# Kernel optimization log

Measured on AMD Instinct MI355X. Metric: run time of the kernel, lower is better.

Reference implementation:

```python
import jax, jax.numpy as jnp
import numpy as np

B, S, D_MODEL, D_K, D_V, H = 4, 2048, 1024, 1024, 1024, 16


def setup_inputs() -> dict:
    key = jax.random.key(0)
    ks = jax.random.split(key, 8)
    std_qk = np.sqrt(2.0 / (D_MODEL + D_K)).astype(np.float32)
    std_v = np.sqrt(2.0 / (D_MODEL + D_V)).astype(np.float32)
    std_o = np.sqrt(2.0 / (D_V + D_MODEL)).astype(np.float32)  # xavier normal
    return {
        "Q": jax.random.normal(ks[0], (B, S, D_MODEL), jnp.float32),
        "K": jax.random.normal(ks[1], (B, S, D_MODEL), jnp.float32),
        "V": jax.random.normal(ks[2], (B, S, D_MODEL), jnp.float32),
        "Wq": jax.random.normal(ks[3], (D_MODEL, D_K), jnp.float32) * std_qk,
        "bq": jnp.zeros((D_K,), jnp.float32),
        "Wk": jax.random.normal(ks[4], (D_MODEL, D_K), jnp.float32) * std_qk,
        "bk": jnp.zeros((D_K,), jnp.float32),
        "Wv": jax.random.normal(ks[5], (D_MODEL, D_V), jnp.float32) * std_v,
        "bv": jnp.zeros((D_V,), jnp.float32),
        "Wo": jax.random.normal(ks[6], (D_V, D_MODEL), jnp.float32) * std_o,
        "bo": jnp.zeros((D_MODEL,), jnp.float32),
    }


def reference(Q, K, V, Wq, bq, Wk, bk, Wv, bv, Wo, bo):
    b, s, _ = Q.shape
    hd = D_K // H  # per-head dim
    # separate QKV projections
    q = (Q @ Wq + bq).reshape(b, s, H, hd)
    k = (K @ Wk + bk).reshape(b, s, H, hd)
    v = (V @ Wv + bv).reshape(b, s, H, D_V // H)
    # scaled dot-product attention per head
    scale = 1.0 / jnp.sqrt(jnp.asarray(hd, Q.dtype))
    scores = jnp.einsum("bqhd,bkhd->bhqk", q, k) * scale
    attn = jax.nn.softmax(scores, axis=-1)
    o = jnp.einsum("bhqk,bkhd->bqhd", attn, v).reshape(b, s, D_V)
    # output projection
    return o @ Wo + bo
```

## Files before the change

kernel.cpp:

```cpp
#include <hip/hip_runtime.h>
#include <hip/hip_bf16.h>
#include <stdint.h>


#define B_  4
#define S_  2048
#define DM  1024
#define H_  16
#define HD  64
#define BH  (B_ * H_)

typedef __attribute__((ext_vector_type(8))) short short8;
typedef __attribute__((ext_vector_type(4))) float f32x4;

union U8 { short8 v; ushort u[8]; };

__device__ __forceinline__ ushort f2bf(float f) {
  union { float f; uint32_t i; } x; x.f = f;
  uint32_t r = (x.i + 0x7FFFu + ((x.i >> 16) & 1u)) >> 16;
  return (ushort)r;
}

__device__ __forceinline__ uint32_t cvt_pk_bf16(float a, float b) {
  uint32_t r;
  asm("v_cvt_pk_bf16_f32 %0, %1, %2" : "=v"(r) : "v"(a), "v"(b));
  return r;
}

__device__ __forceinline__ float exp2f_fast(float x) {
  float r;
  asm("v_exp_f32 %0, %1" : "=v"(r) : "v"(x));
  return r;
}

__device__ __forceinline__ void glds16(const ushort* g, ushort* l) {
  __builtin_amdgcn_global_load_lds(
      (const __attribute__((address_space(1))) void*)g,
      (__attribute__((address_space(3))) void*)l, 16, 0, 0);
}

#define MAX3(a, b, c) fmaxf(fmaxf((a), (b)), (c))

__global__ __launch_bounds__(256) void transposeW4(
    const float* __restrict__ s0, const float* __restrict__ s1,
    const float* __restrict__ s2, const float* __restrict__ s3,
    ushort* __restrict__ dbase) {
  __shared__ __align__(16) ushort tile[64][72];
  const int t = threadIdx.x;
  const int bx = blockIdx.x & 15;
  const int by = blockIdx.x >> 4;
  const int wsel = blockIdx.y;
  const float* src = wsel == 0 ? s0 : (wsel == 1 ? s1 : (wsel == 2 ? s2 : s3));
  ushort* dst = dbase + (size_t)wsel * 1024 * 1024;
#pragma unroll
  for (int i = 0; i < 2; i++) {
    int e = (i * 256 + t) * 8;
    int r = e >> 6, c = e & 63;
    const float* sp = src + (size_t)(by * 64 + r) * 1024 + bx * 64 + c;
    float4 a = ((const float4*)sp)[0];
    float4 b = ((const float4*)sp)[1];
    tile[r][c + 0] = f2bf(a.x); tile[r][c + 1] = f2bf(a.y);
    tile[r][c + 2] = f2bf(a.z); tile[r][c + 3] = f2bf(a.w);
    tile[r][c + 4] = f2bf(b.x); tile[r][c + 5] = f2bf(b.y);
    tile[r][c + 6] = f2bf(b.z); tile[r][c + 7] = f2bf(b.w);
  }
  __syncthreads();
#pragma unroll
  for (int i = 0; i < 2; i++) {
    int e = (i * 256 + t) * 8;
    int r = e >> 6, c = e & 63;
    U8 st;
#pragma unroll
    for (int j = 0; j < 8; j++) st.u[j] = tile[c + j][r];
    *(short8*)(dst + (size_t)(bx * 64 + r) * 1024 + by * 64 + c) = st.v;
  }
}


__global__ __launch_bounds__(256, 2) void gemm_qkv(
    const float* __restrict__ Qa, const float* __restrict__ Ka, const float* __restrict__ Va,
    const ushort* __restrict__ WT,
    const float* __restrict__ bq, const float* __restrict__ bk, const float* __restrict__ bv,
    ushort* __restrict__ qws, ushort* __restrict__ kws, ushort* __restrict__ vt) {
  __shared__ __align__(16) ushort lA[128 * 32];
  __shared__ __align__(16) ushort lB[128 * 32];
  const int z = blockIdx.z;
  const float* Ap = z == 0 ? Qa : (z == 1 ? Ka : Va);
  const ushort* BT = WT + (size_t)z * 1024 * 1024;
  const float* bias = z == 0 ? bq : (z == 1 ? bk : bv);
  const float oscale = z == 0 ? 0.18033688f : 1.0f;
  const int t = threadIdx.x;
  const int lane = t & 63;
  const int w = t >> 6;
  const int wr = w >> 1, wc = w & 1;
  const int bm0 = blockIdx.x * 128;
  const int bn0 = blockIdx.y * 128;
  f32x4 acc[4][4] = {};

  const int arow = t >> 2;
  const int acol = (t & 3) * 8;
  const int swz  = ((t & 3) ^ ((t >> 3) & 3)) * 8;
  const int rdo  = (((lane >> 4) ^ ((lane >> 1) & 3))) * 8;
  const float* fA0 = Ap + (size_t)(bm0 + arow) * 1024 + acol;
  const float* fA1 = Ap + (size_t)(bm0 + 64 + arow) * 1024 + acol;
  const ushort* gB0 = BT + (size_t)(bn0 + arow) * 1024 + swz;
  const ushort* gB1 = BT + (size_t)(bn0 + 64 + arow) * 1024 + swz;
  ushort* lAs0 = &lA[(t >> 2) * 32 + swz];
  ushort* lAs1 = &lA[2048 + (t >> 2) * 32 + swz];

  float4 px0 = ((const float4*)fA0)[0];
  float4 px1 = ((const float4*)fA0)[1];
  float4 py0 = ((const float4*)fA1)[0];
  float4 py1 = ((const float4*)fA1)[1];

  for (int k0 = 0; k0 < 1024; k0 += 32) {
    if (k0) __syncthreads();
    union { short8 v; uint32_t u[4]; } s0, s1;
    s0.u[0] = cvt_pk_bf16(px0.x, px0.y); s0.u[1] = cvt_pk_bf16(px0.z, px0.w);
    s0.u[2] = cvt_pk_bf16(px1.x, px1.y); s0.u[3] = cvt_pk_bf16(px1.z, px1.w);
    s1.u[0] = cvt_pk_bf16(py0.x, py0.y); s1.u[1] = cvt_pk_bf16(py0.z, py0.w);
    s1.u[2] = cvt_pk_bf16(py1.x, py1.y); s1.u[3] = cvt_pk_bf16(py1.z, py1.w);
    *(short8*)lAs0 = s0.v;
    *(short8*)lAs1 = s1.v;
    glds16(gB0 + k0, &lB[t * 8]);
    glds16(gB1 + k0, &lB[2048 + t * 8]);
    __syncthreads();
    if (k0 + 32 < 1024) {
      px0 = ((const float4*)(fA0 + k0 + 32))[0];
      px1 = ((const float4*)(fA0 + k0 + 32))[1];
      py0 = ((const float4*)(fA1 + k0 + 32))[0];
      py1 = ((const float4*)(fA1 + k0 + 32))[1];
    }
    short8 af[4], bf[4];
#pragma unroll
    for (int i = 0; i < 4; i++)
      af[i] = *(const short8*)&lA[(wr * 64 + i * 16 + (lane & 15)) * 32 + rdo];
#pragma unroll
    for (int j = 0; j < 4; j++)
      bf[j] = *(const short8*)&lB[(wc * 64 + j * 16 + (lane & 15)) * 32 + rdo];
#pragma unroll
    for (int i = 0; i < 4; i++)
#pragma unroll
      for (int j = 0; j < 4; j++)
        acc[i][j] = __builtin_amdgcn_mfma_f32_16x16x32_bf16(af[i], bf[j], acc[i][j], 0, 0, 0);
  }

  const int r0 = (lane >> 4) * 4;
#pragma unroll
  for (int j = 0; j < 4; j++) {
    const int col = bn0 + wc * 64 + j * 16 + (lane & 15);
    const float bc = bias[col];
#pragma unroll
    for (int i = 0; i < 4; i++) {
      const int row = bm0 + wr * 64 + i * 16 + r0;
      const int bb = row >> 11, s = row & 2047;
      const int hh = col >> 6, d = col & 63;
      if (z == 2) {
        uint32_t p01 = cvt_pk_bf16(acc[i][j][0] + bc, acc[i][j][1] + bc);
        uint32_t p23 = cvt_pk_bf16(acc[i][j][2] + bc, acc[i][j][3] + bc);
        ushort* vtb = vt + (((size_t)bb * H_ + hh) * HD + d) * (size_t)S_;
        const int sc = (s & 63) >> 2;
        *(uint2*)(vtb + (s & ~63) + ((sc ^ (d & 15)) << 2)) = (uint2){p01, p23};
      } else {
        ushort* dst = z == 0 ? qws : kws;
#pragma unroll
        for (int r = 0; r < 4; r++) {
          float val = (acc[i][j][r] + bc) * oscale;
          dst[(((size_t)bb * H_ + hh) * S_ + (s + r)) * HD + d] = f2bf(val);
        }
      }
    }
  }
}

__global__ __launch_bounds__(256, 2) void gemm_out(
    const ushort* __restrict__ Ap, const ushort* __restrict__ BT,
    const float* __restrict__ bias, float* __restrict__ Cp) {
  __shared__ __align__(16) ushort lA[128 * 32];
  __shared__ __align__(16) ushort lB[128 * 32];
  const int t = threadIdx.x;
  const int lane = t & 63;
  const int w = t >> 6;
  const int wr = w >> 1, wc = w & 1;
  const int bm0 = blockIdx.x * 128;
  const int bn0 = blockIdx.y * 128;
  f32x4 acc[4][4] = {};

  const int arow = t >> 2;
  const int swz  = ((t & 3) ^ ((t >> 3) & 3)) * 8;
  const int rdo  = (((lane >> 4) ^ ((lane >> 1) & 3))) * 8;
  const ushort* gA0 = Ap + (size_t)(bm0 + arow) * 1024 + swz;
  const ushort* gA1 = Ap + (size_t)(bm0 + 64 + arow) * 1024 + swz;
  const ushort* gB0 = BT + (size_t)(bn0 + arow) * 1024 + swz;
  const ushort* gB1 = BT + (size_t)(bn0 + 64 + arow) * 1024 + swz;

  for (int k0 = 0; k0 < 1024; k0 += 32) {
    if (k0) __syncthreads();
    glds16(gA0 + k0, &lA[t * 8]);
    glds16(gA1 + k0, &lA[2048 + t * 8]);
    glds16(gB0 + k0, &lB[t * 8]);
    glds16(gB1 + k0, &lB[2048 + t * 8]);
    __syncthreads();
    short8 af[4], bf[4];
#pragma unroll
    for (int i = 0; i < 4; i++)
      af[i] = *(const short8*)&lA[(wr * 64 + i * 16 + (lane & 15)) * 32 + rdo];
#pragma unroll
    for (int j = 0; j < 4; j++)
      bf[j] = *(const short8*)&lB[(wc * 64 + j * 16 + (lane & 15)) * 32 + rdo];
#pragma unroll
    for (int i = 0; i < 4; i++)
#pragma unroll
      for (int j = 0; j < 4; j++)
        acc[i][j] = __builtin_amdgcn_mfma_f32_16x16x32_bf16(af[i], bf[j], acc[i][j], 0, 0, 0);
  }

  const int r0 = (lane >> 4) * 4;
#pragma unroll
  for (int j = 0; j < 4; j++) {
    const int col = bn0 + wc * 64 + j * 16 + (lane & 15);
    const float bc = bias[col];
#pragma unroll
    for (int i = 0; i < 4; i++) {
      const int row = bm0 + wr * 64 + i * 16 + r0;
#pragma unroll
      for (int r = 0; r < 4; r++)
        Cp[(size_t)(row + r) * 1024 + col] = acc[i][j][r] + bc;
    }
  }
}

__global__ __launch_bounds__(256, 2) void attn(
    const ushort* __restrict__ q, const ushort* __restrict__ k,
    const ushort* __restrict__ vt, ushort* __restrict__ o) {
  __shared__ __align__(16) ushort kbuf[2][4096];
  __shared__ __align__(16) ushort vbuf[2][4096];
  const int t = threadIdx.x;
  const int lane = t & 63;
  const int w = t >> 6;
  const int L = ((blockIdx.x & 7) << 6) + (blockIdx.x >> 3);
  const int bh = L >> 3;
  const int q0 = (L & 7) * 256;
  const int b = bh >> 4, h = bh & 15;
  const int l15 = lane & 15;
  const int g = lane >> 4;

  const ushort* kbase  = k  + (size_t)bh * S_ * HD;
  const ushort* vtbase = vt + (size_t)bh * HD * S_;

  short8 qf[4][2];
#pragma unroll
  for (int qi = 0; qi < 4; qi++) {
    const ushort* qp = q + ((size_t)bh * S_ + q0 + w * 64 + qi * 16 + l15) * HD + g * 8;
    qf[qi][0] = *(const short8*)qp;
    qf[qi][1] = *(const short8*)(qp + 32);
  }

  short8 onesf;
#pragma unroll
  for (int j = 0; j < 8; j++) onesf[j] = (short)0x3F80;

  float m_r[4] = {0.f, 0.f, 0.f, 0.f};
  f32x4 l_acc[4];
  f32x4 o_acc[4][4];
#pragma unroll
  for (int qi = 0; qi < 4; qi++) {
    l_acc[qi] = (f32x4){0.f, 0.f, 0.f, 0.f};
#pragma unroll
    for (int cb = 0; cb < 4; cb++) o_acc[qi][cb] = (f32x4){0.f, 0.f, 0.f, 0.f};
  }

  int vo[2][2];
#pragma unroll
  for (int ks = 0; ks < 2; ks++) {
    vo[ks][0] = ((8 * ks + g) ^ l15) << 2;
    vo[ks][1] = ((8 * ks + 4 + g) ^ l15) << 2;
  }

  const int c0 = t, c1 = 256 + t;
  const int kr0 = c0 >> 3, kc0 = c0 & 7;
  const int kr1 = c1 >> 3, kc1 = c1 & 7;
  const int kp0 = (c0 & ~7) | (kc0 ^ (kr0 & 7));
  const int kp1 = (c1 & ~7) | (kc1 ^ (kr1 & 7));
  const ushort* gk0 = kbase + (size_t)kr0 * HD + kc0 * 8;
  const ushort* gk1 = kbase + (size_t)kr1 * HD + kc1 * 8;
  const ushort* gv0 = vtbase + (size_t)kr0 * S_ + kc0 * 8;
  const ushort* gv1 = vtbase + (size_t)kr1 * S_ + kc1 * 8;
  uint4 rk0, rk1, rv0, rv1;
  auto LOADR = [&](int kv0) {
    rk0 = *(const uint4*)(gk0 + (size_t)kv0 * HD);
    rk1 = *(const uint4*)(gk1 + (size_t)kv0 * HD);
    rv0 = *(const uint4*)(gv0 + kv0);
    rv1 = *(const uint4*)(gv1 + kv0);
  };
  auto WRITE = [&](int sel_) {
    *(uint4*)&kbuf[sel_][kp0 * 8] = rk0;
    *(uint4*)&kbuf[sel_][kp1 * 8] = rk1;
    *(uint4*)&vbuf[sel_][c0 * 8] = rv0;
    *(uint4*)&vbuf[sel_][c1 * 8] = rv1;
  };

  LOADR(0);
  WRITE(0);
  __syncthreads();

  int sel = 0;
  for (int kv0 = 0; kv0 < S_; kv0 += 64, sel ^= 1) {
    const int more = (kv0 + 64 < S_);
    if (more) LOADR(kv0 + 64);

    f32x4 sc[4][4];
#pragma unroll
    for (int qi = 0; qi < 4; qi++)
#pragma unroll
      for (int cb = 0; cb < 4; cb++) sc[qi][cb] = (f32x4){0.f, 0.f, 0.f, 0.f};
#pragma unroll
    for (int cb = 0; cb < 4; cb++) {
      const int row = cb * 16 + l15;
      const int r7 = row & 7;
      short8 kf0 = *(const short8*)&kbuf[sel][(row * 8 + (g ^ r7)) * 8];
      short8 kf1 = *(const short8*)&kbuf[sel][(row * 8 + ((4 + g) ^ r7)) * 8];
#pragma unroll
      for (int qi = 0; qi < 4; qi++) {
        sc[qi][cb] = __builtin_amdgcn_mfma_f32_16x16x32_bf16(kf0, qf[qi][0], sc[qi][cb], 0, 0, 0);
        sc[qi][cb] = __builtin_amdgcn_mfma_f32_16x16x32_bf16(kf1, qf[qi][1], sc[qi][cb], 0, 0, 0);
      }
    }

    union PB { short8 v; uint32_t u[4]; } pbq[4][2];
    float mxv[4];
#pragma unroll
    for (int qi = 0; qi < 4; qi++) {
      const float m = m_r[qi];
#pragma unroll
      for (int cb = 0; cb < 4; cb++) {
        float p0 = exp2f_fast(sc[qi][cb][0] - m);
        float p1 = exp2f_fast(sc[qi][cb][1] - m);
        float p2 = exp2f_fast(sc[qi][cb][2] - m);
        float p3 = exp2f_fast(sc[qi][cb][3] - m);
        pbq[qi][cb >> 1].u[(cb & 1) * 2 + 0] = cvt_pk_bf16(p0, p1);
        pbq[qi][cb >> 1].u[(cb & 1) * 2 + 1] = cvt_pk_bf16(p2, p3);
      }
      float z0 = MAX3(sc[qi][0][0], sc[qi][0][1], sc[qi][0][2]);
      float z1 = MAX3(sc[qi][0][3], sc[qi][1][0], sc[qi][1][1]);
      float z2 = MAX3(sc[qi][1][2], sc[qi][1][3], sc[qi][2][0]);
      float z3 = MAX3(sc[qi][2][1], sc[qi][2][2], sc[qi][2][3]);
      float z4 = MAX3(sc[qi][3][0], sc[qi][3][1], sc[qi][3][2]);
      mxv[qi] = MAX3(MAX3(z0, z1, z2), fmaxf(z3, z4), sc[qi][3][3]);
    }

#pragma unroll
    for (int ks = 0; ks < 2; ks++) {
#pragma unroll
      for (int qi = 0; qi < 4; qi++)
        l_acc[qi] = __builtin_amdgcn_mfma_f32_16x16x32_bf16(onesf, pbq[qi][ks].v, l_acc[qi], 0, 0, 0);
#pragma unroll
      for (int cb = 0; cb < 4; cb++) {
        const ushort* vb = &vbuf[sel][(cb * 16 + l15) * 64];
        union { short8 v; uint2 d2[2]; } vv;
        vv.d2[0] = *(const uint2*)(vb + vo[ks][0]);
        vv.d2[1] = *(const uint2*)(vb + vo[ks][1]);
#pragma unroll
        for (int qi = 0; qi < 4; qi++)
          o_acc[qi][cb] = __builtin_amdgcn_mfma_f32_16x16x32_bf16(vv.v, pbq[qi][ks].v, o_acc[qi][cb], 0, 0, 0);
      }
    }

#pragma unroll
    for (int qi = 0; qi < 4; qi++) {
      float mx = mxv[qi];
      mx = fmaxf(mx, __shfl_xor(mx, 16));
      mx = fmaxf(mx, __shfl_xor(mx, 32));
      const float THR = 11.5415603f;
      const float m = m_r[qi];
      if (!__all(mx <= m + THR)) {
        float mn = fmaxf(m, mx);
        float fct = exp2f_fast(m - mn);
        m_r[qi] = mn;
        l_acc[qi] *= fct;
#pragma unroll
        for (int cb = 0; cb < 4; cb++)
#pragma unroll
          for (int rr = 0; rr < 4; rr++) o_acc[qi][cb][rr] *= fct;
      }
    }

    if (more) WRITE(sel ^ 1);
    __syncthreads();
  }

#pragma unroll
  for (int qi = 0; qi < 4; qi++) {
    const float inv = 1.f / l_acc[qi][0];
    ushort* ob = o + ((size_t)b * S_ + q0 + w * 64 + qi * 16 + l15) * DM + h * HD + 4 * g;
#pragma unroll
    for (int cb = 0; cb < 4; cb++) {
      uint2 st;
      st.x = cvt_pk_bf16(o_acc[qi][cb][0] * inv, o_acc[qi][cb][1] * inv);
      st.y = cvt_pk_bf16(o_acc[qi][cb][2] * inv, o_acc[qi][cb][3] * inv);
      *(uint2*)(ob + cb * 16) = st;
    }
  }
}

extern "C" void kernel_launch(void* const* d_in, const int* in_sizes, int n_in,
                              void* d_out, int out_size, void* d_ws, size_t ws_size,
                              hipStream_t stream) {
  const float* Q  = (const float*)d_in[0];
  const float* K  = (const float*)d_in[1];
  const float* V  = (const float*)d_in[2];
  const float* Wq = (const float*)d_in[3];
  const float* bq = (const float*)d_in[4];
  const float* Wk = (const float*)d_in[5];
  const float* bk = (const float*)d_in[6];
  const float* Wv = (const float*)d_in[7];
  const float* bv = (const float*)d_in[8];
  const float* Wo = (const float*)d_in[9];
  const float* bo = (const float*)d_in[10];
  float* out = (float*)d_out;
  ushort* ws = (ushort*)d_ws;

  const size_t WN = (size_t)1024 * 1024;
  const size_t PN = (size_t)B_ * S_ * DM;
  ushort* wT  = ws;
  ushort* woT = ws + 3 * WN;
  ushort* qws = ws + 4 * WN;
  ushort* kws = qws + PN;
  ushort* ows = kws + PN;
  ushort* vt  = (ushort*)d_out;

  transposeW4<<<dim3(256, 4), 256, 0, stream>>>(Wq, Wk, Wv, Wo, wT);

  gemm_qkv<<<dim3(64, 8, 3), 256, 0, stream>>>(Q, K, V, wT, bq, bk, bv, qws, kws, vt);

  attn<<<BH * 8, 256, 0, stream>>>(qws, kws, vt, ows);

  gemm_out<<<dim3(64, 8), 256, 0, stream>>>(ows, woT, bo, out);
}
```

Before: 195.8 us.

## Register-prefetch A tile in output GEMM and fold max into score init

```diff
diff --git a/kernel.cpp b/kernel.cpp
--- a/kernel.cpp
+++ b/kernel.cpp
@@ -187,20 +187,30 @@
   f32x4 acc[4][4] = {};
 
   const int arow = t >> 2;
+  const int acol = (t & 3) * 8;
   const int swz  = ((t & 3) ^ ((t >> 3) & 3)) * 8;
   const int rdo  = (((lane >> 4) ^ ((lane >> 1) & 3))) * 8;
-  const ushort* gA0 = Ap + (size_t)(bm0 + arow) * 1024 + swz;
-  const ushort* gA1 = Ap + (size_t)(bm0 + 64 + arow) * 1024 + swz;
+  const ushort* gA0 = Ap + (size_t)(bm0 + arow) * 1024 + acol;
+  const ushort* gA1 = Ap + (size_t)(bm0 + 64 + arow) * 1024 + acol;
   const ushort* gB0 = BT + (size_t)(bn0 + arow) * 1024 + swz;
   const ushort* gB1 = BT + (size_t)(bn0 + 64 + arow) * 1024 + swz;
+  ushort* lAs0 = &lA[(t >> 2) * 32 + swz];
+  ushort* lAs1 = &lA[2048 + (t >> 2) * 32 + swz];
+
+  short8 ra0 = *(const short8*)gA0;
+  short8 ra1 = *(const short8*)gA1;
 
   for (int k0 = 0; k0 < 1024; k0 += 32) {
     if (k0) __syncthreads();
-    glds16(gA0 + k0, &lA[t * 8]);
-    glds16(gA1 + k0, &lA[2048 + t * 8]);
+    *(short8*)lAs0 = ra0;
+    *(short8*)lAs1 = ra1;
     glds16(gB0 + k0, &lB[t * 8]);
     glds16(gB1 + k0, &lB[2048 + t * 8]);
     __syncthreads();
+    if (k0 + 32 < 1024) {
+      ra0 = *(const short8*)(gA0 + k0 + 32);
+      ra1 = *(const short8*)(gA1 + k0 + 32);
+    }
     short8 af[4], bf[4];
 #pragma unroll
     for (int i = 0; i < 4; i++)
@@ -311,9 +321,11 @@
 
     f32x4 sc[4][4];
 #pragma unroll
-    for (int qi = 0; qi < 4; qi++)
-#pragma unroll
-      for (int cb = 0; cb < 4; cb++) sc[qi][cb] = (f32x4){0.f, 0.f, 0.f, 0.f};
+    for (int qi = 0; qi < 4; qi++) {
+      const float nm = -m_r[qi];
+#pragma unroll
+      for (int cb = 0; cb < 4; cb++) sc[qi][cb] = (f32x4){nm, nm, nm, nm};
+    }
 #pragma unroll
     for (int cb = 0; cb < 4; cb++) {
       const int row = cb * 16 + l15;
@@ -331,13 +343,12 @@
     float mxv[4];
 #pragma unroll
     for (int qi = 0; qi < 4; qi++) {
-      const float m = m_r[qi];
 #pragma unroll
       for (int cb = 0; cb < 4; cb++) {
-        float p0 = exp2f_fast(sc[qi][cb][0] - m);
-        float p1 = exp2f_fast(sc[qi][cb][1] - m);
-        float p2 = exp2f_fast(sc[qi][cb][2] - m);
-        float p3 = exp2f_fast(sc[qi][cb][3] - m);
+        float p0 = exp2f_fast(sc[qi][cb][0]);
+        float p1 = exp2f_fast(sc[qi][cb][1]);
+        float p2 = exp2f_fast(sc[qi][cb][2]);
+        float p3 = exp2f_fast(sc[qi][cb][3]);
         pbq[qi][cb >> 1].u[(cb & 1) * 2 + 0] = cvt_pk_bf16(p0, p1);
         pbq[qi][cb >> 1].u[(cb & 1) * 2 + 1] = cvt_pk_bf16(p2, p3);
       }
@@ -372,11 +383,10 @@
       mx = fmaxf(mx, __shfl_xor(mx, 16));
       mx = fmaxf(mx, __shfl_xor(mx, 32));
       const float THR = 11.5415603f;
-      const float m = m_r[qi];
-      if (!__all(mx <= m + THR)) {
-        float mn = fmaxf(m, mx);
-        float fct = exp2f_fast(m - mn);
-        m_r[qi] = mn;
+      if (!__all(mx <= THR)) {
+        float d = fmaxf(mx, 0.f);
+        float fct = exp2f_fast(-d);
+        m_r[qi] += d;
         l_acc[qi] *= fct;
 #pragma unroll
         for (int cb = 0; cb < 4; cb++)
```

Result: no change. 191.9 us, median of 2 (-2.0%).
